# Performance work log

Hardware: AMD Instinct MI355X
Metric: run time of the kernel (lower is better)

## Reference

```python
import jax, jax.numpy as jnp
import numpy as np

VOCAB, EMB, HDIM, VDIM, ATT = 30000, 256, 512, 128, 256
B, N, T = 64, 196, 32


def setup_inputs() -> dict:
    key = jax.random.key(0)
    ks = jax.random.split(key, 8)
    s = 0.02
    return {
        "V": jax.random.normal(ks[0], (B, N, VDIM), jnp.float32),
        "y": jax.random.randint(ks[1], (B, T), 0, VOCAB),
        "embed": jax.random.normal(ks[2], (VOCAB, EMB), jnp.float32) * s,
        "att_W_w": jax.random.normal(ks[3], (ATT, HDIM), jnp.float32) * s,
        "att_W_b": jnp.zeros((ATT,), jnp.float32),
        "att_U_w": jax.random.normal(ks[4], (ATT, VDIM), jnp.float32) * s,
        "att_U_b": jnp.zeros((ATT,), jnp.float32),
        "att_v_w": jax.random.normal(ks[5], (1, ATT), jnp.float32) * s,
        "att_v_b": jnp.zeros((1,), jnp.float32),
        "W_ih": jax.random.normal(ks[6], (4 * HDIM, EMB + VDIM), jnp.float32) * s,
        "W_hh": jax.random.normal(ks[7], (4 * HDIM, HDIM), jnp.float32) * s,
        "b_ih": jnp.zeros((4 * HDIM,), jnp.float32),
        "b_hh": jnp.zeros((4 * HDIM,), jnp.float32),
        "proj_w": jax.random.normal(jax.random.fold_in(key, 9), (EMB, HDIM), jnp.float32) * s,
    }


def reference(V, y, embed, att_W_w, att_W_b, att_U_w, att_U_b, att_v_w, att_v_b,
              W_ih, W_hh, b_ih, b_hh, proj_w):
    Bsz = y.shape[0]
    hdim = W_hh.shape[1]
    # loop-invariant U(V): [B, N, ATT]
    UV = jnp.einsum('bnv,av->bna', V, att_U_w) + att_U_b

    def step(carry, y_t):
        h, c, x_t = carry
        # additive attention
        Wh = h @ att_W_w.T + att_W_b                      # [B, ATT]
        e = jnp.tanh(Wh[:, None, :] + UV) @ att_v_w.T + att_v_b  # [B, N, 1]
        a = jax.nn.softmax(e, axis=1)
        ctx = jnp.sum(a * V, axis=1)                      # [B, VDIM]
        # LSTMCell (PyTorch gate order i, f, g, o)
        xc = jnp.concatenate([x_t, ctx], axis=-1)
        gates = xc @ W_ih.T + b_ih + h @ W_hh.T + b_hh
        i, f, g, o = jnp.split(gates, 4, axis=-1)
        c_new = jax.nn.sigmoid(f) * c + jax.nn.sigmoid(i) * jnp.tanh(g)
        h_new = jax.nn.sigmoid(o) * jnp.tanh(c_new)
        # dropout is identity in eval mode
        e_t = h_new @ proj_w.T                            # [B, EMB]
        logit = e_t @ embed.T                             # [B, VOCAB]
        x_next = embed[y_t]                               # teacher forcing
        return (h_new, c_new, x_next), logit

    h0 = jnp.zeros((Bsz, hdim), V.dtype)
    c0 = jnp.zeros((Bsz, hdim), V.dtype)
    x0 = embed[y[:, 0]]
    _, logits = jax.lax.scan(step, (h0, c0, x0), y[:, 1:].T)  # [T-1, B, VOCAB]
    return jnp.transpose(logits, (1, 0, 2))
```

## Files before the change

kernel.cpp:

```cpp
#include <hip/hip_runtime.h>
#include <stdint.h>

typedef unsigned short u16;
typedef uint32_t u32;
typedef short s16x8 __attribute__((ext_vector_type(8)));
typedef float f32x4 __attribute__((ext_vector_type(4)));

#define DEV __device__ __forceinline__

#define TSCALE 2.885390082f

DEV float bf2f(u16 h){ union{u32 u; float f;} x; x.u = ((u32)h)<<16; return x.f; }
DEV u16 f2bf(float f){ union{float f; u32 u;} x; x.f = f; u32 u = x.u;
  return (u16)((u + 0x7fffu + ((u>>16)&1u))>>16); }
DEV float bflo(u32 w){ union{u32 u; float f;} x; x.u = w<<16; return x.f; }
DEV float bfhi(u32 w){ union{u32 u; float f;} x; x.u = w & 0xffff0000u; return x.f; }

DEV float exp2_fast(float x){ return __builtin_amdgcn_exp2f(x); }
DEV float rcp_fast(float x){ return __builtin_amdgcn_rcpf(x); }
DEV float tanh2(float x){ float t = exp2_fast(TSCALE*x);
  return fmaf(-2.f, rcp_fast(t + 1.f), 1.f); }
DEV float sig2(float x){ return rcp_fast(1.f + exp2_fast(-1.442695041f*x)); }

DEV u32   ld_u(const u32* p){ return __hip_atomic_load(p, __ATOMIC_RELAXED, __HIP_MEMORY_SCOPE_AGENT); }
DEV void  st_u(u32* p, u32 v){ __hip_atomic_store(p, v, __ATOMIC_RELAXED, __HIP_MEMORY_SCOPE_AGENT); }

__global__ void f2b_kernel(const float* __restrict__ src, u16* __restrict__ dst, int n4, float scale){
  int i = blockIdx.x*blockDim.x + threadIdx.x;
  if (i < n4) {
    float4 v = ((const float4*)src)[i];
    ushort4 o; o.x = f2bf(v.x*scale); o.y = f2bf(v.y*scale); o.z = f2bf(v.z*scale); o.w = f2bf(v.w*scale);
    ((ushort4*)dst)[i] = o;
  }
}

__global__ void prep_wih2b(const float* __restrict__ Wih, u16* __restrict__ Wc){
  int idx = blockIdx.x*256 + threadIdx.x;
  int j = idx>>7, k = idx&127;
  Wc[idx] = f2bf(Wih[(size_t)j*384 + 256 + k]);
}

__global__ void repack_h(const u16* __restrict__ H2, u16* __restrict__ Hl){
  int r = blockIdx.x;
  int s = r>>6, b = r&63;
  int tid = threadIdx.x;
  u32 v = *((const u32*)(H2 + (size_t)(s+1)*32768 + (size_t)(tid>>2)*512 + (size_t)b*8) + (tid&3));
  ((u32*)(Hl + (size_t)r*512))[tid] = v;
}

__global__ __launch_bounds__(256) void gemm_bt(
    const u16* __restrict__ A, int lda,
    const u16* __restrict__ B, int ldb,
    const float* __restrict__ bias1, const float* __restrict__ bias2, float bscale,
    void* __restrict__ C, int ldc,
    int M, int N, int K, int Mt, int mode)
{
  __shared__ __align__(16) u16 As[64*64];
  __shared__ __align__(16) u16 Bs[128*64];
  int nwg = (int)gridDim.x;
  int b0 = blockIdx.x;
  int qq = nwg >> 3, rr = nwg & 7;
  int bswz;
  if (qq == 0) bswz = b0;
  else {
    int xcd = b0 & 7, i = b0 >> 3;
    bswz = (xcd < rr) ? (xcd*(qq+1) + i) : (rr*(qq+1) + (xcd - rr)*qq + i);
  }
  int mt = bswz % Mt, nt = bswz / Mt;
  int m0 = mt*64, n0 = nt*128;
  int tid = threadIdx.x, wave = tid>>6, lane = tid&63;
  int lrow = lane>>3, lcol = (lane&7)*8;
  f32x4 acc[2][4];
  #pragma unroll
  for (int i=0;i<2;i++)
    #pragma unroll
    for (int j=0;j<4;j++) acc[i][j] = (f32x4){0,0,0,0};
  int wm = (wave>>1)*32, wn = (wave&1)*64;
  int fr = lane&15, fk = (lane>>4)*8;
  for (int k0 = 0; k0 < K; k0 += 64) {
    __syncthreads();
    #pragma unroll
    for (int i = 0; i < 2; i++) {
      int ci = wave + i*4;
      int row = ci*8 + lrow;
      const u16* g = A + (size_t)(m0+row)*lda + k0 + lcol;
      __builtin_amdgcn_global_load_lds(
        (const __attribute__((address_space(1))) u32*)g,
        (__attribute__((address_space(3))) u32*)&As[ci*512], 16, 0, 0);
    }
    #pragma unroll
    for (int i = 0; i < 4; i++) {
      int ci = wave + i*4;
      int row = ci*8 + lrow;
      int gr = n0 + row; gr = gr < N ? gr : N-1;
      const u16* g = B + (size_t)gr*ldb + k0 + lcol;
      __builtin_amdgcn_global_load_lds(
        (const __attribute__((address_space(1))) u32*)g,
        (__attribute__((address_space(3))) u32*)&Bs[ci*512], 16, 0, 0);
    }
    __syncthreads();
    #pragma unroll
    for (int kk = 0; kk < 2; kk++) {
      s16x8 af[2], bfv[4];
      #pragma unroll
      for (int mi=0; mi<2; mi++)
        af[mi] = *(const s16x8*)&As[(wm + mi*16 + fr)*64 + kk*32 + fk];
      #pragma unroll
      for (int ni=0; ni<4; ni++)
        bfv[ni] = *(const s16x8*)&Bs[(wn + ni*16 + fr)*64 + kk*32 + fk];
      #pragma unroll
      for (int mi=0; mi<2; mi++)
        #pragma unroll
        for (int ni=0; ni<4; ni++)
          acc[mi][ni] = __builtin_amdgcn_mfma_f32_16x16x32_bf16(af[mi], bfv[ni], acc[mi][ni], 0,0,0);
    }
  }
  #pragma unroll
  for (int mi=0; mi<2; mi++)
    #pragma unroll
    for (int ni=0; ni<4; ni++) {
      int col = n0 + wn + ni*16 + (lane&15);
      if (col >= N) continue;
      float bv = 0.0f;
      if (bias1) bv += bias1[col];
      if (bias2) bv += bias2[col];
      bv *= bscale;
      int rbase = m0 + wm + mi*16 + ((lane>>4)<<2);
      #pragma unroll
      for (int r=0; r<4; r++) {
        int row = rbase + r;
        float v = acc[mi][ni][r] + bv;
        if (mode == 0) ((float*)C)[(size_t)row*ldc + col] = v;
        else if (mode == 1) ((u16*)C)[(size_t)row*ldc + col] = f2bf(v);
        else { int orow = (row&63)*31 + (row>>6); ((float*)C)[(size_t)orow*ldc + col] = v; }
      }
    }
}

__global__ void gather_x(const int* __restrict__ y, const float* __restrict__ embed, u16* __restrict__ X)
{
  int r = blockIdx.x;
  int s = r>>6, b = r&63;
  int tok = y[b*32 + s];
  X[(size_t)r*256 + threadIdx.x] = f2bf(embed[(size_t)tok*256 + threadIdx.x]);
}

#define NB 64

DEV void gbar(u32* flags, int bid, unsigned g){
  __asm__ volatile("" ::: "memory");
  __builtin_amdgcn_s_waitcnt(0);
  __syncthreads();
  if (threadIdx.x == 0) st_u(&flags[bid*16], g);
  if (threadIdx.x < 64) {
    for (;;) {
      u32 a = ld_u(&flags[threadIdx.x*16]);
      if (__all(a >= g)) break;
      __builtin_amdgcn_s_sleep(1);
    }
  }
  __syncthreads();
  __asm__ volatile("" ::: "memory");
}

__global__ __launch_bounds__(512, 1) void decoder_steps(
    const float* __restrict__ V,
    const float* __restrict__ attWb,
    const float* __restrict__ attvw,
    const float* __restrict__ attvb,
    const u16* __restrict__ WhhB,
    const u16* __restrict__ attWwB,
    const u16* __restrict__ WcB,
    u16* __restrict__ H2,
    const u16* __restrict__ UV,
    const u16* __restrict__ Xg,
    u16* __restrict__ CtxB,
    u32* __restrict__ flags)
{
  int bid = blockIdx.x, tid = threadIdx.x;
  int wave = tid>>6, lane = tid&63;
  int fr = lane&15, fkq = lane>>4;

  __shared__ __align__(16) u16 Wlds[32][648];
  __shared__ __align__(16) u16 Xglds[64][32];
  __shared__ float hls[512];
  __shared__ float whs[256];
  __shared__ float vws[256];
  __shared__ float esc[200];
  __shared__ float red1;
  __shared__ float part[512];

  {
    int r = tid>>4, p = tid&15;
    int grow = ((r>>3)<<9) + bid*8 + (r&7);
    #pragma unroll
    for (int i=0;i<5;i++){
      int k = p*40 + i*8;
      const u16* src = (k < 512) ? (WhhB + (size_t)grow*512 + k)
                                 : (WcB  + (size_t)grow*128 + (k-512));
      *(s16x8*)&Wlds[r][k] = *(const s16x8*)src;
    }
  }
  if (tid < 256) vws[tid] = attvw[tid];
  float vb = attvb[0];
  float c_reg[4] = {0.f,0.f,0.f,0.f};
  unsigned gen = 0;
  __syncthreads();

  int br = wave*16 + fr;

  for (int t = 0; t < 31; t++) {
    s16x8 af[16];
    s16x8 xg;
    if (tid < 256) {
      const u16* Hbase = H2 + (size_t)t*32768 + (size_t)br*8;
      #pragma unroll
      for (int kt=0;kt<16;kt++) af[kt] = *(const s16x8*)(Hbase + (size_t)(kt*4+fkq)*512);
    } else {
      int t2 = tid - 256;
      u32 hv = *((const u32*)(H2 + (size_t)t*32768 + (size_t)(t2>>2)*512 + (size_t)bid*8) + (t2&3));
      hls[2*t2]   = bflo(hv);
      hls[2*t2+1] = bfhi(hv);
      xg = *(const s16x8*)(Xg + (size_t)t*131072 + (size_t)(t2>>2)*2048 + (size_t)(t2&3)*512 + (size_t)bid*8);
    }
    __syncthreads();

    {
      int a_ = tid>>1, kh = (tid&1)*256;
      const u32* wr = (const u32*)(attWwB + (size_t)a_*512 + kh);
      float acc = (tid&1) ? 0.f : TSCALE * attWb[a_];
      #pragma unroll 4
      for (int k=0;k<256;k+=8){
        u32 w0 = wr[(k>>1)+0], w1 = wr[(k>>1)+1], w2 = wr[(k>>1)+2], w3 = wr[(k>>1)+3];
        float4 h0 = *(const float4*)&hls[kh+k];
        float4 h1 = *(const float4*)&hls[kh+k+4];
        acc = fmaf(bflo(w0), h0.x, acc); acc = fmaf(bfhi(w0), h0.y, acc);
        acc = fmaf(bflo(w1), h0.z, acc); acc = fmaf(bfhi(w1), h0.w, acc);
        acc = fmaf(bflo(w2), h1.x, acc); acc = fmaf(bfhi(w2), h1.y, acc);
        acc = fmaf(bflo(w3), h1.z, acc); acc = fmaf(bfhi(w3), h1.w, acc);
      }
      acc += __shfl_xor(acc, 1);
      if (!(tid&1)) whs[a_] = acc;
    }

    f32x4 a0 = (f32x4){0,0,0,0}, a1 = (f32x4){0,0,0,0};
    if (tid < 256) {
      #pragma unroll
      for (int kt=0;kt<16;kt++){
        s16x8 b0 = *(const s16x8*)&Wlds[fr][kt*32 + fkq*8];
        s16x8 b1 = *(const s16x8*)&Wlds[16+fr][kt*32 + fkq*8];
        a0 = __builtin_amdgcn_mfma_f32_16x16x32_bf16(af[kt], b0, a0, 0,0,0);
        a1 = __builtin_amdgcn_mfma_f32_16x16x32_bf16(af[kt], b1, a1, 0,0,0);
      }
      __builtin_amdgcn_sched_barrier(0);
    }
    __syncthreads();

    if (tid < 392) {
      int n = tid>>1, kh = (tid&1)*128;
      const u32* uvp = (const u32*)(UV + ((size_t)bid*196 + n)*256 + kh);
      float e0 = 0.0f, e1 = 0.0f;
      #pragma unroll 4
      for (int a = 0; a < 128; a += 4) {
        u32 uw0 = uvp[(a>>1)], uw1 = uvp[(a>>1)+1];
        float4 w4 = *(const float4*)&whs[kh+a];
        float4 v4 = *(const float4*)&vws[kh+a];
        float t0 = exp2_fast(w4.x + bflo(uw0));
        float t1 = exp2_fast(w4.y + bfhi(uw0));
        float t2 = exp2_fast(w4.z + bflo(uw1));
        float t3 = exp2_fast(w4.w + bfhi(uw1));
        e0 = fmaf(v4.x, fmaf(-2.f, rcp_fast(t0+1.f), 1.f), e0);
        e1 = fmaf(v4.y, fmaf(-2.f, rcp_fast(t1+1.f), 1.f), e1);
        e0 = fmaf(v4.z, fmaf(-2.f, rcp_fast(t2+1.f), 1.f), e0);
        e1 = fmaf(v4.w, fmaf(-2.f, rcp_fast(t3+1.f), 1.f), e1);
      }
      float e = e0 + e1;
      e += __shfl_xor(e, 1);
      if (!(tid&1)) esc[n] = exp2_fast(1.442695041f*(e + vb));
    }
    if (tid >= 256) {
      int t2 = tid - 256;
      *(s16x8*)&Xglds[t2>>2][(t2&3)*8] = xg;
    }
    __syncthreads();

    if (tid < 64) {
      float s = esc[tid] + esc[64+tid] + esc[128+tid];
      if (tid < 4)  s += esc[192+tid];
      #pragma unroll
      for (int off=32; off>=1; off>>=1) s += __shfl_xor(s, off);
      if (tid==0) red1 = s;
    }
    {
      int k = tid&127, q4 = tid>>7;
      const float* vp = V + ((size_t)bid*196 + q4*49)*128 + k;
      float a = 0.f;
      for (int n2=0; n2<49; n2++) a = fmaf(esc[q4*49+n2], vp[(size_t)n2*128], a);
      part[tid] = a;
    }
    __syncthreads();

    if (tid < 64) {
      float inv = rcp_fast(red1);
      float c0 = (part[2*tid]   + part[128+2*tid] + part[256+2*tid] + part[384+2*tid]) * inv;
      float c1 = (part[2*tid+1] + part[129+2*tid] + part[257+2*tid] + part[385+2*tid]) * inv;
      u32 pk = (u32)f2bf(c0) | ((u32)f2bf(c1) << 16);
      st_u((u32*)(CtxB + (size_t)t*8192 + (size_t)bid*128) + tid, pk);
    }
    gen++; gbar(flags, bid, gen);

    if (tid < 256) {
      const u16* Crow = CtxB + (size_t)t*8192 + (size_t)br*128 + fkq*8;
      #pragma unroll
      for (int kt=0;kt<4;kt++){
        s16x8 cf = *(const s16x8*)(Crow + kt*32);
        s16x8 b0 = *(const s16x8*)&Wlds[fr][(16+kt)*32 + fkq*8];
        s16x8 b1 = *(const s16x8*)&Wlds[16+fr][(16+kt)*32 + fkq*8];
        a0 = __builtin_amdgcn_mfma_f32_16x16x32_bf16(cf, b0, a0, 0,0,0);
        a1 = __builtin_amdgcn_mfma_f32_16x16x32_bf16(cf, b1, a1, 0,0,0);
      }
      int c = fr;
      int xr0 = ((c>>3)&1)*8 + (c&7);
      float v0[4], v1[4], s0[4], s1[4];
      #pragma unroll
      for (int r=0;r<4;r++){
        int b_r = wave*16 + fkq*4 + r;
        v0[r] = a0[r] + bf2f(Xglds[b_r][xr0]);
        v1[r] = a1[r] + bf2f(Xglds[b_r][16+xr0]);
      }
      #pragma unroll
      for (int r=0;r<4;r++){ s0[r] = __shfl_xor(v0[r], 8); s1[r] = __shfl_xor(v1[r], 8); }
      if (c < 8) {
        #pragma unroll
        for (int r=0;r<4;r++){
          int b_r = wave*16 + fkq*4 + r;
          float ig = sig2(v0[r]);
          float fg = sig2(s0[r]);
          float gg = tanh2(v1[r]);
          float og = sig2(s1[r]);
          float cn = fmaf(fg, c_reg[r], ig*gg);
          c_reg[r] = cn;
          float hvv = og * tanh2(cn);
          float hp = __shfl_xor(hvv, 1);
          if (!(c&1)) {
            u32 pk = (u32)f2bf(hvv) | ((u32)f2bf(hp) << 16);
            st_u((u32*)(H2 + (size_t)(t+1)*32768 + (size_t)bid*512 + (size_t)b_r*8) + (c>>1), pk);
          }
        }
      }
    }
    if (t < 30) { gen++; gbar(flags, bid, gen); }
  }
}

#define OFF_H    1024u
#define OFF_UV   2098176u
#define OFF_X    8520704u
#define OFF_XG   9536512u
#define OFF_GH   17662976u
#define OFF_EMB  OFF_GH
#define OFF_WH   33915904u
#define OFF_E    35947520u
#define OFF_VB   36963328u
#define OFF_WIH  40174592u
#define OFF_WHH  41747456u
#define OFF_AWW  43844608u
#define OFF_AUW  44106752u
#define OFF_PRJ  44172288u

extern "C" void kernel_launch(void* const* d_in, const int* in_sizes, int n_in,
                              void* d_out, int out_size, void* d_ws, size_t ws_size,
                              hipStream_t stream)
{
  const float* V      = (const float*)d_in[0];
  const int*   y      = (const int*)  d_in[1];
  const float* embed  = (const float*)d_in[2];
  const float* attWw  = (const float*)d_in[3];
  const float* attWb  = (const float*)d_in[4];
  const float* attUw  = (const float*)d_in[5];
  const float* attUb  = (const float*)d_in[6];
  const float* attvw  = (const float*)d_in[7];
  const float* attvb  = (const float*)d_in[8];
  const float* Wih    = (const float*)d_in[9];
  const float* Whh    = (const float*)d_in[10];
  const float* bih    = (const float*)d_in[11];
  const float* bhh    = (const float*)d_in[12];
  const float* projw  = (const float*)d_in[13];
  float* out = (float*)d_out;
  char* ws = (char*)d_ws;

  u16*   H2   = (u16*)  (ws + OFF_H);
  u16*   UVb  = (u16*)  (ws + OFF_UV);
  u16*   Xb   = (u16*)  (ws + OFF_X);
  u16*   Xg   = (u16*)  (ws + OFF_XG);
  u16*   Hl   = (u16*)  (ws + OFF_XG);
  u32*   flags= (u32*)  (ws + OFF_WH);
  u16*   CtxB = (u16*)  (ws + OFF_WH + 8192);
  u16*   E    = (u16*)  (ws + OFF_E);
  u16*   Vb   = (u16*)  (ws + OFF_VB);
  u16*   WcB  = (u16*)  (ws + OFF_VB);
  u16*   embB = (u16*)  (ws + OFF_EMB);
  u16*   WihB = (u16*)  (ws + OFF_WIH);
  u16*   WhhB = (u16*)  (ws + OFF_WHH);
  u16*   attWwB = (u16*)(ws + OFF_AWW);
  u16*   attUwB = (u16*)(ws + OFF_AUW);
  u16*   projB  = (u16*)(ws + OFF_PRJ);

  hipMemsetAsync(ws + OFF_H, 0, 65536, stream);
  hipMemsetAsync(ws + OFF_WH, 0, 4096, stream);

  f2b_kernel<<<(401408+255)/256, 256, 0, stream>>>(V,     Vb,     401408, 1.0f);
  f2b_kernel<<<(196608+255)/256, 256, 0, stream>>>(Wih,   WihB,   196608, 1.0f);
  f2b_kernel<<<(262144+255)/256, 256, 0, stream>>>(Whh,   WhhB,   262144, 1.0f);
  f2b_kernel<<<(32768+255)/256,  256, 0, stream>>>(attWw, attWwB,  32768, TSCALE);
  f2b_kernel<<<(8192+255)/256,   256, 0, stream>>>(attUw, attUwB,   8192, TSCALE);
  f2b_kernel<<<(32768+255)/256,  256, 0, stream>>>(projw, projB,   32768, 1.0f);
  f2b_kernel<<<(1920000+255)/256, 256, 0, stream>>>(embed, embB, 1920000, 1.0f);

  gather_x<<<1984, 256, 0, stream>>>(y, embed, Xb);

  gemm_bt<<<196*2, 256, 0, stream>>>(Vb, 128, attUwB, 128, attUb, nullptr, TSCALE,
                                     UVb, 256, 12544, 256, 128, 196, 1);
  prep_wih2b<<<1024, 256, 0, stream>>>(Wih, WcB);
  gemm_bt<<<31*16, 256, 0, stream>>>(Xb, 256, WihB, 384, bih, bhh, 1.0f,
                                     Xg, 2048, 1984, 2048, 256, 31, 1);

  decoder_steps<<<NB, 512, 0, stream>>>(V, attWb, attvw, attvb,
      WhhB, attWwB, WcB, H2, UVb, Xg, CtxB, flags);

  repack_h<<<1984, 256, 0, stream>>>(H2, Hl);

  gemm_bt<<<31*2, 256, 0, stream>>>(Hl, 512, projB, 512, nullptr, nullptr, 1.0f,
                                    E, 256, 1984, 256, 512, 31, 1);
  gemm_bt<<<31*235, 256, 0, stream>>>(E, 256, embB, 256, nullptr, nullptr, 1.0f,
                                      out, 30000, 1984, 30000, 256, 31, 2);
}
```

Measured before the change: 968.5 us.

## Split LSTM gate MFMAs across all eight waves and fuse prep kernels

The recurrent gate matmul now uses all eight waves instead of four. Each wave holds its W_hh/W_c slice as register-resident B fragments rather than reading them from LDS, and gate results go through a small LDS tile so every thread does one cell's LSTM update. The seven conversion kernels and the embedding gather are merged into one launch to cut launch overhead. Register pressure rises (20 fragment registers plus 16 H fragments), and launch_bounds changes to 2 blocks per SM.

```diff
diff --git a/kernel.cpp b/kernel.cpp
--- a/kernel.cpp
+++ b/kernel.cpp
@@ -25,12 +25,32 @@
 DEV u32   ld_u(const u32* p){ return __hip_atomic_load(p, __ATOMIC_RELAXED, __HIP_MEMORY_SCOPE_AGENT); }
 DEV void  st_u(u32* p, u32 v){ __hip_atomic_store(p, v, __ATOMIC_RELAXED, __HIP_MEMORY_SCOPE_AGENT); }
 
-__global__ void f2b_kernel(const float* __restrict__ src, u16* __restrict__ dst, int n4, float scale){
-  int i = blockIdx.x*blockDim.x + threadIdx.x;
-  if (i < n4) {
-    float4 v = ((const float4*)src)[i];
-    ushort4 o; o.x = f2bf(v.x*scale); o.y = f2bf(v.y*scale); o.z = f2bf(v.z*scale); o.w = f2bf(v.w*scale);
-    ((ushort4*)dst)[i] = o;
+DEV void cvt4(const float* __restrict__ src, u16* __restrict__ dst, int i, float scale){
+  float4 v = ((const float4*)src)[i];
+  ushort4 o; o.x = f2bf(v.x*scale); o.y = f2bf(v.y*scale); o.z = f2bf(v.z*scale); o.w = f2bf(v.w*scale);
+  ((ushort4*)dst)[i] = o;
+}
+__global__ void prep_all(
+    const float* __restrict__ V, const float* __restrict__ Wih, const float* __restrict__ Whh,
+    const float* __restrict__ attWw, const float* __restrict__ attUw, const float* __restrict__ projw,
+    const float* __restrict__ embed, const int* __restrict__ y,
+    u16* __restrict__ Vb, u16* __restrict__ WihB, u16* __restrict__ WhhB,
+    u16* __restrict__ attWwB, u16* __restrict__ attUwB, u16* __restrict__ projB,
+    u16* __restrict__ embB, u16* __restrict__ Xb)
+{
+  int blk = blockIdx.x, tid = threadIdx.x;
+  if      (blk < 1568)  cvt4(V,     Vb,     blk*256 + tid, 1.0f);
+  else if (blk < 2336)  cvt4(Wih,   WihB,   (blk-1568)*256 + tid, 1.0f);
+  else if (blk < 3360)  cvt4(Whh,   WhhB,   (blk-2336)*256 + tid, 1.0f);
+  else if (blk < 3488)  cvt4(attWw, attWwB, (blk-3360)*256 + tid, TSCALE);
+  else if (blk < 3520)  cvt4(attUw, attUwB, (blk-3488)*256 + tid, TSCALE);
+  else if (blk < 3648)  cvt4(projw, projB,  (blk-3520)*256 + tid, 1.0f);
+  else if (blk < 11148) cvt4(embed, embB,   (blk-3648)*256 + tid, 1.0f);
+  else {
+    int r = blk - 11148;
+    int s = r>>6, b = r&63;
+    int tok = y[b*32 + s];
+    Xb[(size_t)r*256 + tid] = f2bf(embed[(size_t)tok*256 + tid]);
   }
 }
 
@@ -137,14 +157,6 @@
     }
 }
 
-__global__ void gather_x(const int* __restrict__ y, const float* __restrict__ embed, u16* __restrict__ X)
-{
-  int r = blockIdx.x;
-  int s = r>>6, b = r&63;
-  int tok = y[b*32 + s];
-  X[(size_t)r*256 + threadIdx.x] = f2bf(embed[(size_t)tok*256 + threadIdx.x]);
-}
-
 #define NB 64
 
 DEV void gbar(u32* flags, int bid, unsigned g){
@@ -163,7 +175,7 @@
   __asm__ volatile("" ::: "memory");
 }
 
-__global__ __launch_bounds__(512, 1) void decoder_steps(
+__global__ __launch_bounds__(512, 2) void decoder_steps(
     const float* __restrict__ V,
     const float* __restrict__ attWb,
     const float* __restrict__ attvw,
@@ -180,48 +192,48 @@
   int bid = blockIdx.x, tid = threadIdx.x;
   int wave = tid>>6, lane = tid&63;
   int fr = lane&15, fkq = lane>>4;
-
-  __shared__ __align__(16) u16 Wlds[32][648];
-  __shared__ __align__(16) u16 Xglds[64][32];
+  int gsel = wave&1, bsel = wave>>1;
+  int b2 = tid>>3, dd = tid&7;
+
   __shared__ float hls[512];
   __shared__ float whs[256];
   __shared__ float vws[256];
   __shared__ float esc[200];
   __shared__ float red1;
   __shared__ float part[512];
-
-  {
-    int r = tid>>4, p = tid&15;
-    int grow = ((r>>3)<<9) + bid*8 + (r&7);
-    #pragma unroll
-    for (int i=0;i<5;i++){
-      int k = p*40 + i*8;
-      const u16* src = (k < 512) ? (WhhB + (size_t)grow*512 + k)
-                                 : (WcB  + (size_t)grow*128 + (k-512));
-      *(s16x8*)&Wlds[r][k] = *(const s16x8*)src;
-    }
-  }
+  __shared__ float glds[64][36];
+
+  int r32 = gsel*16 + fr;
+  int grow = ((r32>>3)<<9) + bid*8 + (r32&7);
+  s16x8 bfrag[20];
+  #pragma unroll
+  for (int kt=0;kt<16;kt++)
+    bfrag[kt] = *(const s16x8*)&WhhB[(size_t)grow*512 + kt*32 + fkq*8];
+  #pragma unroll
+  for (int kt=0;kt<4;kt++)
+    bfrag[16+kt] = *(const s16x8*)&WcB[(size_t)grow*128 + kt*32 + fkq*8];
+
   if (tid < 256) vws[tid] = attvw[tid];
   float vb = attvb[0];
-  float c_reg[4] = {0.f,0.f,0.f,0.f};
+  float c_reg = 0.f;
   unsigned gen = 0;
   __syncthreads();
 
-  int br = wave*16 + fr;
+  int br = bsel*16 + fr;
 
   for (int t = 0; t < 31; t++) {
     s16x8 af[16];
-    s16x8 xg;
-    if (tid < 256) {
-      const u16* Hbase = H2 + (size_t)t*32768 + (size_t)br*8;
-      #pragma unroll
-      for (int kt=0;kt<16;kt++) af[kt] = *(const s16x8*)(Hbase + (size_t)(kt*4+fkq)*512);
-    } else {
+    const u16* Hbase = H2 + (size_t)t*32768 + (size_t)br*8;
+    #pragma unroll
+    for (int kt=0;kt<16;kt++) af[kt] = *(const s16x8*)(Hbase + (size_t)(kt*4+fkq)*512);
+    u16 xr0, xr1, xr2, xr3;
+    { const u16* xp = Xg + (size_t)t*131072 + (size_t)b2*2048 + bid*8 + dd;
+      xr0 = xp[0]; xr1 = xp[512]; xr2 = xp[1024]; xr3 = xp[1536]; }
+    if (tid >= 256) {
       int t2 = tid - 256;
       u32 hv = *((const u32*)(H2 + (size_t)t*32768 + (size_t)(t2>>2)*512 + (size_t)bid*8) + (t2&3));
       hls[2*t2]   = bflo(hv);
       hls[2*t2+1] = bfhi(hv);
-      xg = *(const s16x8*)(Xg + (size_t)t*131072 + (size_t)(t2>>2)*2048 + (size_t)(t2&3)*512 + (size_t)bid*8);
     }
     __syncthreads();
 
@@ -243,17 +255,11 @@
       if (!(tid&1)) whs[a_] = acc;
     }
 
-    f32x4 a0 = (f32x4){0,0,0,0}, a1 = (f32x4){0,0,0,0};
-    if (tid < 256) {
-      #pragma unroll
-      for (int kt=0;kt<16;kt++){
-        s16x8 b0 = *(const s16x8*)&Wlds[fr][kt*32 + fkq*8];
-        s16x8 b1 = *(const s16x8*)&Wlds[16+fr][kt*32 + fkq*8];
-        a0 = __builtin_amdgcn_mfma_f32_16x16x32_bf16(af[kt], b0, a0, 0,0,0);
-        a1 = __builtin_amdgcn_mfma_f32_16x16x32_bf16(af[kt], b1, a1, 0,0,0);
-      }
-      __builtin_amdgcn_sched_barrier(0);
-    }
+    f32x4 a0 = (f32x4){0,0,0,0};
+    #pragma unroll
+    for (int kt=0;kt<16;kt++)
+      a0 = __builtin_amdgcn_mfma_f32_16x16x32_bf16(af[kt], bfrag[kt], a0, 0,0,0);
+    __builtin_amdgcn_sched_barrier(0);
     __syncthreads();
 
     if (tid < 392) {
@@ -278,10 +284,6 @@
       e += __shfl_xor(e, 1);
       if (!(tid&1)) esc[n] = exp2_fast(1.442695041f*(e + vb));
     }
-    if (tid >= 256) {
-      int t2 = tid - 256;
-      *(s16x8*)&Xglds[t2>>2][(t2&3)*8] = xg;
-    }
     __syncthreads();
 
     if (tid < 64) {
@@ -309,44 +311,31 @@
     }
     gen++; gbar(flags, bid, gen);
 
-    if (tid < 256) {
+    {
       const u16* Crow = CtxB + (size_t)t*8192 + (size_t)br*128 + fkq*8;
       #pragma unroll
       for (int kt=0;kt<4;kt++){
         s16x8 cf = *(const s16x8*)(Crow + kt*32);
-        s16x8 b0 = *(const s16x8*)&Wlds[fr][(16+kt)*32 + fkq*8];
-        s16x8 b1 = *(const s16x8*)&Wlds[16+fr][(16+kt)*32 + fkq*8];
-        a0 = __builtin_amdgcn_mfma_f32_16x16x32_bf16(cf, b0, a0, 0,0,0);
-        a1 = __builtin_amdgcn_mfma_f32_16x16x32_bf16(cf, b1, a1, 0,0,0);
+        a0 = __builtin_amdgcn_mfma_f32_16x16x32_bf16(cf, bfrag[16+kt], a0, 0,0,0);
       }
-      int c = fr;
-      int xr0 = ((c>>3)&1)*8 + (c&7);
-      float v0[4], v1[4], s0[4], s1[4];
-      #pragma unroll
-      for (int r=0;r<4;r++){
-        int b_r = wave*16 + fkq*4 + r;
-        v0[r] = a0[r] + bf2f(Xglds[b_r][xr0]);
-        v1[r] = a1[r] + bf2f(Xglds[b_r][16+xr0]);
-      }
-      #pragma unroll
-      for (int r=0;r<4;r++){ s0[r] = __shfl_xor(v0[r], 8); s1[r] = __shfl_xor(v1[r], 8); }
-      if (c < 8) {
-        #pragma unroll
-        for (int r=0;r<4;r++){
-          int b_r = wave*16 + fkq*4 + r;
-          float ig = sig2(v0[r]);
-          float fg = sig2(s0[r]);
-          float gg = tanh2(v1[r]);
-          float og = sig2(s1[r]);
-          float cn = fmaf(fg, c_reg[r], ig*gg);
-          c_reg[r] = cn;
-          float hvv = og * tanh2(cn);
-          float hp = __shfl_xor(hvv, 1);
-          if (!(c&1)) {
-            u32 pk = (u32)f2bf(hvv) | ((u32)f2bf(hp) << 16);
-            st_u((u32*)(H2 + (size_t)(t+1)*32768 + (size_t)bid*512 + (size_t)b_r*8) + (c>>1), pk);
-          }
-        }
+      #pragma unroll
+      for (int r=0;r<4;r++)
+        glds[bsel*16 + fkq*4 + r][r32] = a0[r];
+    }
+    __syncthreads();
+
+    {
+      float xi = glds[b2][dd]      + bf2f(xr0);
+      float xf = glds[b2][8+dd]    + bf2f(xr1);
+      float xg = glds[b2][16+dd]   + bf2f(xr2);
+      float xo = glds[b2][24+dd]   + bf2f(xr3);
+      float cn = fmaf(sig2(xf), c_reg, sig2(xi)*tanh2(xg));
+      c_reg = cn;
+      float hv = sig2(xo)*tanh2(cn);
+      float hp = __shfl_xor(hv, 1);
+      if (!(dd&1)) {
+        u32 pk = (u32)f2bf(hv) | ((u32)f2bf(hp) << 16);
+        st_u((u32*)(H2 + (size_t)(t+1)*32768 + (size_t)bid*512 + (size_t)b2*8) + (dd>>1), pk);
       }
     }
     if (t < 30) { gen++; gbar(flags, bid, gen); }
@@ -409,15 +398,8 @@
   hipMemsetAsync(ws + OFF_H, 0, 65536, stream);
   hipMemsetAsync(ws + OFF_WH, 0, 4096, stream);
 
-  f2b_kernel<<<(401408+255)/256, 256, 0, stream>>>(V,     Vb,     401408, 1.0f);
-  f2b_kernel<<<(196608+255)/256, 256, 0, stream>>>(Wih,   WihB,   196608, 1.0f);
-  f2b_kernel<<<(262144+255)/256, 256, 0, stream>>>(Whh,   WhhB,   262144, 1.0f);
-  f2b_kernel<<<(32768+255)/256,  256, 0, stream>>>(attWw, attWwB,  32768, TSCALE);
-  f2b_kernel<<<(8192+255)/256,   256, 0, stream>>>(attUw, attUwB,   8192, TSCALE);
-  f2b_kernel<<<(32768+255)/256,  256, 0, stream>>>(projw, projB,   32768, 1.0f);
-  f2b_kernel<<<(1920000+255)/256, 256, 0, stream>>>(embed, embB, 1920000, 1.0f);
-
-  gather_x<<<1984, 256, 0, stream>>>(y, embed, Xb);
+  prep_all<<<13132, 256, 0, stream>>>(V, Wih, Whh, attWw, attUw, projw, embed, y,
+                                      Vb, WihB, WhhB, attWwB, attUwB, projB, embB, Xb);
 
   gemm_bt<<<196*2, 256, 0, stream>>>(Vb, 128, attUwB, 128, attUb, nullptr, TSCALE,
                                      UVb, 256, 12544, 256, 128, 196, 1);
```

Result: slower. 1.000 ms (+3.3%).

## Fuse prep conversions into one launch and keep embedding tile resident for logits

Applied to the files above, without the earlier changes.

Merges the seven fp32-to-bf16 conversion launches and the token gather into a single kernel, which removes launch overhead. Replaces the generic logits GEMM with a kernel in which each block keeps a 128-column slice of the bf16 embedding (K=256) resident in LDS and loops over all 31 row tiles of E, so the embedding matrix is read from memory only once. The trade-off is that only 235 blocks run, fewer than the generic GEMM launched, so occupancy and per-block serial work may become the limit. Stores go directly to the transposed [B,T-1,VOCAB] output layout.

```diff
diff --git a/kernel.cpp b/kernel.cpp
--- a/kernel.cpp
+++ b/kernel.cpp
@@ -25,12 +25,32 @@
 DEV u32   ld_u(const u32* p){ return __hip_atomic_load(p, __ATOMIC_RELAXED, __HIP_MEMORY_SCOPE_AGENT); }
 DEV void  st_u(u32* p, u32 v){ __hip_atomic_store(p, v, __ATOMIC_RELAXED, __HIP_MEMORY_SCOPE_AGENT); }
 
-__global__ void f2b_kernel(const float* __restrict__ src, u16* __restrict__ dst, int n4, float scale){
-  int i = blockIdx.x*blockDim.x + threadIdx.x;
-  if (i < n4) {
-    float4 v = ((const float4*)src)[i];
-    ushort4 o; o.x = f2bf(v.x*scale); o.y = f2bf(v.y*scale); o.z = f2bf(v.z*scale); o.w = f2bf(v.w*scale);
-    ((ushort4*)dst)[i] = o;
+DEV void cvt4(const float* __restrict__ src, u16* __restrict__ dst, int i, float scale){
+  float4 v = ((const float4*)src)[i];
+  ushort4 o; o.x = f2bf(v.x*scale); o.y = f2bf(v.y*scale); o.z = f2bf(v.z*scale); o.w = f2bf(v.w*scale);
+  ((ushort4*)dst)[i] = o;
+}
+__global__ void prep_all(
+    const float* __restrict__ V, const float* __restrict__ Wih, const float* __restrict__ Whh,
+    const float* __restrict__ attWw, const float* __restrict__ attUw, const float* __restrict__ projw,
+    const float* __restrict__ embed, const int* __restrict__ y,
+    u16* __restrict__ Vb, u16* __restrict__ WihB, u16* __restrict__ WhhB,
+    u16* __restrict__ attWwB, u16* __restrict__ attUwB, u16* __restrict__ projB,
+    u16* __restrict__ embB, u16* __restrict__ Xb)
+{
+  int blk = blockIdx.x, tid = threadIdx.x;
+  if      (blk < 1568)  cvt4(V,     Vb,     blk*256 + tid, 1.0f);
+  else if (blk < 2336)  cvt4(Wih,   WihB,   (blk-1568)*256 + tid, 1.0f);
+  else if (blk < 3360)  cvt4(Whh,   WhhB,   (blk-2336)*256 + tid, 1.0f);
+  else if (blk < 3488)  cvt4(attWw, attWwB, (blk-3360)*256 + tid, TSCALE);
+  else if (blk < 3520)  cvt4(attUw, attUwB, (blk-3488)*256 + tid, TSCALE);
+  else if (blk < 3648)  cvt4(projw, projB,  (blk-3520)*256 + tid, 1.0f);
+  else if (blk < 11148) cvt4(embed, embB,   (blk-3648)*256 + tid, 1.0f);
+  else {
+    int r = blk - 11148;
+    int s = r>>6, b = r&63;
+    int tok = y[b*32 + s];
+    Xb[(size_t)r*256 + tid] = f2bf(embed[(size_t)tok*256 + tid]);
   }
 }
 
@@ -137,12 +157,71 @@
     }
 }
 
-__global__ void gather_x(const int* __restrict__ y, const float* __restrict__ embed, u16* __restrict__ X)
+__global__ __launch_bounds__(256) void logits_nstat(
+    const u16* __restrict__ E,
+    const u16* __restrict__ Bm,
+    float* __restrict__ C)
 {
-  int r = blockIdx.x;
-  int s = r>>6, b = r&63;
-  int tok = y[b*32 + s];
-  X[(size_t)r*256 + threadIdx.x] = f2bf(embed[(size_t)tok*256 + threadIdx.x]);
+  __shared__ __align__(16) u16 Bs[4096*8];
+  __shared__ __align__(16) u16 As[2048*8];
+  int tid = threadIdx.x, wave = tid>>6, lane = tid&63;
+  int fr = lane&15, fkq = lane>>4;
+  int n0 = blockIdx.x*128;
+  for (int j=0;j<16;j++){
+    int e = wave*16 + j;
+    int c = e>>1, r0 = (e&1)*64;
+    int gr = n0 + r0 + lane; if (gr > 29999) gr = 29999;
+    const u16* g = Bm + (size_t)gr*256 + c*8;
+    __builtin_amdgcn_global_load_lds(
+      (const __attribute__((address_space(1))) u32*)g,
+      (__attribute__((address_space(3))) u32*)&Bs[((size_t)c*128 + r0)*8], 16, 0, 0);
+  }
+  f32x4 acc[4][2];
+  for (int mt=0; mt<31; mt++){
+    __syncthreads();
+    #pragma unroll
+    for (int j=0;j<8;j++){
+      int c = wave*8 + j;
+      const u16* g = E + (size_t)(mt*64 + lane)*256 + c*8;
+      __builtin_amdgcn_global_load_lds(
+        (const __attribute__((address_space(1))) u32*)g,
+        (__attribute__((address_space(3))) u32*)&As[((size_t)c*64 + lane)*8], 16, 0, 0);
+    }
+    __syncthreads();
+    #pragma unroll
+    for (int mi=0;mi<4;mi++)
+      #pragma unroll
+      for (int ni=0;ni<2;ni++) acc[mi][ni]=(f32x4){0,0,0,0};
+    #pragma unroll
+    for (int kk=0;kk<8;kk++){
+      int c = kk*4 + fkq;
+      s16x8 bfv[2], af[4];
+      #pragma unroll
+      for (int ni=0;ni<2;ni++)
+        bfv[ni] = *(const s16x8*)&Bs[((size_t)c*128 + wave*32 + ni*16 + fr)*8];
+      #pragma unroll
+      for (int mi=0;mi<4;mi++)
+        af[mi] = *(const s16x8*)&As[((size_t)c*64 + mi*16 + fr)*8];
+      #pragma unroll
+      for (int mi=0;mi<4;mi++)
+        #pragma unroll
+        for (int ni=0;ni<2;ni++)
+          acc[mi][ni] = __builtin_amdgcn_mfma_f32_16x16x32_bf16(af[mi], bfv[ni], acc[mi][ni], 0,0,0);
+    }
+    #pragma unroll
+    for (int mi=0;mi<4;mi++)
+      #pragma unroll
+      for (int ni=0;ni<2;ni++){
+        int col = n0 + wave*32 + ni*16 + fr;
+        if (col < 30000){
+          #pragma unroll
+          for (int r=0;r<4;r++){
+            int lm = mi*16 + fkq*4 + r;
+            C[(size_t)(lm*31 + mt)*30000 + col] = acc[mi][ni][r];
+          }
+        }
+      }
+  }
 }
 
 #define NB 64
@@ -409,15 +488,8 @@
   hipMemsetAsync(ws + OFF_H, 0, 65536, stream);
   hipMemsetAsync(ws + OFF_WH, 0, 4096, stream);
 
-  f2b_kernel<<<(401408+255)/256, 256, 0, stream>>>(V,     Vb,     401408, 1.0f);
-  f2b_kernel<<<(196608+255)/256, 256, 0, stream>>>(Wih,   WihB,   196608, 1.0f);
-  f2b_kernel<<<(262144+255)/256, 256, 0, stream>>>(Whh,   WhhB,   262144, 1.0f);
-  f2b_kernel<<<(32768+255)/256,  256, 0, stream>>>(attWw, attWwB,  32768, TSCALE);
-  f2b_kernel<<<(8192+255)/256,   256, 0, stream>>>(attUw, attUwB,   8192, TSCALE);
-  f2b_kernel<<<(32768+255)/256,  256, 0, stream>>>(projw, projB,   32768, 1.0f);
-  f2b_kernel<<<(1920000+255)/256, 256, 0, stream>>>(embed, embB, 1920000, 1.0f);
-
-  gather_x<<<1984, 256, 0, stream>>>(y, embed, Xb);
+  prep_all<<<13132, 256, 0, stream>>>(V, Wih, Whh, attWw, attUw, projw, embed, y,
+                                      Vb, WihB, WhhB, attWwB, attUwB, projB, embB, Xb);
 
   gemm_bt<<<196*2, 256, 0, stream>>>(Vb, 128, attUwB, 128, attUb, nullptr, TSCALE,
                                      UVb, 256, 12544, 256, 128, 196, 1);
@@ -432,6 +504,5 @@
 
   gemm_bt<<<31*2, 256, 0, stream>>>(Hl, 512, projB, 512, nullptr, nullptr, 1.0f,
                                     E, 256, 1984, 256, 512, 31, 1);
-  gemm_bt<<<31*235, 256, 0, stream>>>(E, 256, embB, 256, nullptr, nullptr, 1.0f,
-                                      out, 30000, 1984, 30000, 256, 31, 2);
-}
+  logits_nstat<<<235, 256, 0, stream>>>(E, embB, out);
+}
```

Result: no change. 959.3 us (-0.9%).
